# Optimization experiments

Measured on AMD Instinct MI355X. Metric: run time of the kernel, lower is better.

## Reference

```python
import jax, jax.numpy as jnp
import numpy as np


def _wkv_scan(key, value, time_decay, time_first):
    # Numerically-stabilized RWKV WKV recurrence; key/value: [B,T,C]
    w = -jnp.exp(time_decay)  # [C]
    B, T, C = key.shape

    def step(carry, kv):
        num, den, mx = carry
        k, v = kv  # [B,C] each
        # output at this timestep
        mo = jnp.maximum(mx, k + time_first)
        e1 = jnp.exp(mx - mo)
        e2 = jnp.exp(k + time_first - mo)
        out = (e1 * num + e2 * v) / (e1 * den + e2)
        # state update
        ms = jnp.maximum(mx + w, k)
        e1s = jnp.exp(mx + w - ms)
        e2s = jnp.exp(k - ms)
        return (e1s * num + e2s * v, e1s * den + e2s, ms), out

    init = (jnp.zeros((B, C), key.dtype),
            jnp.zeros((B, C), key.dtype),
            jnp.full((B, C), -1e38, key.dtype))
    kT = jnp.swapaxes(key, 0, 1)   # [T,B,C]
    vT = jnp.swapaxes(value, 0, 1)
    _, outs = jax.lax.scan(step, init, (kT, vT))
    return jnp.swapaxes(outs, 0, 1)  # [B,T,C]


def setup_inputs() -> dict:
    key = jax.random.key(0)
    ks = jax.random.split(key, 10)
    B, T, C = 8, 2048, 1024
    s = 1.0 / np.sqrt(C)
    return {
        "x": jax.random.normal(ks[0], (B, T, C), jnp.float32),
        "wk": jax.random.normal(ks[1], (C, C), jnp.float32) * s,
        "wv": jax.random.normal(ks[2], (C, C), jnp.float32) * s,
        "wr": jax.random.normal(ks[3], (C, C), jnp.float32) * s,
        "wo": jax.random.normal(ks[4], (C, C), jnp.float32) * s,
        "time_decay": jax.random.normal(ks[5], (C,), jnp.float32) * 0.5,
        "time_first": jax.random.normal(ks[6], (C,), jnp.float32) * 0.5,
        "mix_k": jax.random.uniform(ks[7], (1, 1, C), jnp.float32),
        "mix_v": jax.random.uniform(ks[8], (1, 1, C), jnp.float32),
        "mix_r": jax.random.uniform(ks[9], (1, 1, C), jnp.float32),
    }


def reference(x, wk, wv, wr, wo, time_decay, time_first, mix_k, mix_v, mix_r):
    # time_shift: prev_x[:,0]=0, prev_x[:,t]=x[:,t-1]  (ZeroPad2d((0,0,1,-1)))
    prev_x = jnp.pad(x, ((0, 0), (1, 0), (0, 0)))[:, :-1, :]
    k_in = x * mix_k + prev_x * (1.0 - mix_k)
    v_in = x * mix_v + prev_x * (1.0 - mix_v)
    r_in = x * mix_r + prev_x * (1.0 - mix_r)
    key = jnp.einsum('btc,dc->btd', k_in, wk)
    value = jnp.einsum('btc,dc->btd', v_in, wv)
    receptance = jax.nn.sigmoid(jnp.einsum('btc,dc->btd', r_in, wr))
    wkv = _wkv_scan(key, value, time_decay, time_first)
    rwkv = receptance * wkv
    return jnp.einsum('btc,dc->btd', rwkv, wo)
```

## Files before the change

kernel.cpp:

```cpp
#include <hip/hip_runtime.h>
#include <stdint.h>


using bf16x8 = __attribute__((ext_vector_type(8))) __bf16;
using f32x4  = __attribute__((ext_vector_type(4))) float;

union FU { float f; unsigned int u; };

__device__ __forceinline__ unsigned short f2b(float f) {
  FU v; v.f = f;
  unsigned int u = v.u;
  return (unsigned short)((u + 0x7fffu + ((u >> 16) & 1u)) >> 16);
}
__device__ __forceinline__ float b2f(unsigned short h) {
  FU v; v.u = ((unsigned int)h) << 16; return v.f;
}

__device__ __forceinline__ void gl_lds16(const unsigned short* g,
                                         const unsigned short* l) {
  __builtin_amdgcn_global_load_lds(
      (const __attribute__((address_space(1))) void*)g,
      (__attribute__((address_space(3))) void*)l, 16, 0, 0);
}

#define SBAR()  asm volatile("s_barrier" ::: "memory")
#define LGKMSOFT() asm volatile("s_waitcnt lgkmcnt(0)" ::: "memory")
#define VMW(n)  asm volatile("s_waitcnt vmcnt(" #n ")" ::: "memory")

__global__ __launch_bounds__(256) void prep_kernel(
    const float* __restrict__ x,
    const float* __restrict__ w0, const float* __restrict__ w1,
    const float* __restrict__ w2, const float* __restrict__ w3,
    unsigned short* __restrict__ o0, unsigned short* __restrict__ o1,
    unsigned short* __restrict__ o2, unsigned short* __restrict__ o3,
    const float* __restrict__ mk, const float* __restrict__ mv,
    const float* __restrict__ mr,
    unsigned short* __restrict__ ok, unsigned short* __restrict__ ov,
    unsigned short* __restrict__ orr, int T, int C)
{
  int bid = blockIdx.x;
  if (bid < 4096) {
    int mat = bid >> 10, blk = bid & 1023;
    const float* src = (mat == 0) ? w0 : (mat == 1) ? w1 : (mat == 2) ? w2 : w3;
    unsigned short* dst = (mat == 0) ? o0 : (mat == 1) ? o1 : (mat == 2) ? o2 : o3;
    int i = blk * 1024 + threadIdx.x * 4;
    float4 v = *(const float4*)(src + i);
    union { int2 i2; unsigned short u[4]; } o;
    o.u[0] = f2b(v.x); o.u[1] = f2b(v.y); o.u[2] = f2b(v.z); o.u[3] = f2b(v.w);
    *(int2*)(dst + i) = o.i2;
    return;
  }
  int i = (bid - 4096) * 256 + threadIdx.x;
  int base = i * 8;
  int row = base / C;
  int t = row - (row / T) * T;
  int c = base - row * C;
  float xv[8], pv[8];
  *(float4*)&xv[0] = *(const float4*)(x + base);
  *(float4*)&xv[4] = *(const float4*)(x + base + 4);
  if (t > 0) {
    *(float4*)&pv[0] = *(const float4*)(x + base - C);
    *(float4*)&pv[4] = *(const float4*)(x + base - C + 4);
  } else {
#pragma unroll
    for (int e = 0; e < 8; ++e) pv[e] = 0.f;
  }
  float mkv[8], mvv[8], mrv[8];
  *(float4*)&mkv[0] = *(const float4*)(mk + c);
  *(float4*)&mkv[4] = *(const float4*)(mk + c + 4);
  *(float4*)&mvv[0] = *(const float4*)(mv + c);
  *(float4*)&mvv[4] = *(const float4*)(mv + c + 4);
  *(float4*)&mrv[0] = *(const float4*)(mr + c);
  *(float4*)&mrv[4] = *(const float4*)(mr + c + 4);
  union { int4 i4; unsigned short u[8]; } a, b2, d;
#pragma unroll
  for (int e = 0; e < 8; ++e) {
    float xe = xv[e], pe = pv[e];
    a.u[e]  = f2b(xe * mkv[e] + pe * (1.f - mkv[e]));
    b2.u[e] = f2b(xe * mvv[e] + pe * (1.f - mvv[e]));
    d.u[e]  = f2b(xe * mrv[e] + pe * (1.f - mrv[e]));
  }
  *(int4*)(ok + base)  = a.i4;
  *(int4*)(ov + base)  = b2.i4;
  *(int4*)(orr + base) = d.i4;
}


__device__ __forceinline__ void stageHalf(
    const unsigned short* __restrict__ g,
    const unsigned short* l,
    int rh, int kt, int w, int rl, int koffel)
{
#pragma unroll
  for (int c = 0; c < 2; ++c) {
    int rows = rh * 128 + (2 * w + c) * 8;
    gl_lds16(g + (size_t)(rows + rl) * 1024 + kt * 64 + koffel,
             l + rows * 64);
  }
}

template<int Q>
__device__ __forceinline__ void quadMfma(f32x4 (&acc)[8][4],
    bf16x8 a00, bf16x8 a01, bf16x8 a10, bf16x8 a11, bf16x8 (&b)[4][2])
{
#pragma unroll
  for (int j = 0; j < 4; ++j) {
    acc[2*Q][j]   = __builtin_amdgcn_mfma_f32_16x16x32_bf16(a00, b[j][0], acc[2*Q][j],   0, 0, 0);
    acc[2*Q][j]   = __builtin_amdgcn_mfma_f32_16x16x32_bf16(a01, b[j][1], acc[2*Q][j],   0, 0, 0);
    acc[2*Q+1][j] = __builtin_amdgcn_mfma_f32_16x16x32_bf16(a10, b[j][0], acc[2*Q+1][j], 0, 0, 0);
    acc[2*Q+1][j] = __builtin_amdgcn_mfma_f32_16x16x32_bf16(a11, b[j][1], acc[2*Q+1][j], 0, 0, 0);
  }
}

template<bool ST_A, bool ST_B, int VMN>
__device__ __forceinline__ void ktile(
    const unsigned short* aR, const unsigned short* bR,
    const unsigned short* aW, const unsigned short* bW,
    const unsigned short* Am, const unsigned short* Wn,
    int ktA, int ktB, int w, int wm, int wn, int col, int quad,
    int swzel, int rl, int koffel, f32x4 (&acc)[8][4])
{
  const int ks0 = (quad * 8) ^ swzel;
  const int ks1 = (32 + quad * 8) ^ swzel;
  bf16x8 b[4][2];
#pragma unroll
  for (int j = 0; j < 4; ++j) {
    const unsigned short* br = bR + (wn * 64 + j * 16 + col) * 64;
    b[j][0] = *(const bf16x8*)(br + ks0);
    b[j][1] = *(const bf16x8*)(br + ks1);
  }
  const unsigned short* ar = aR + (wm * 128 + col) * 64;
  {
    bf16x8 a00 = *(const bf16x8*)(ar + 0 * 1024 + ks0);
    bf16x8 a01 = *(const bf16x8*)(ar + 0 * 1024 + ks1);
    bf16x8 a10 = *(const bf16x8*)(ar + 1 * 1024 + ks0);
    bf16x8 a11 = *(const bf16x8*)(ar + 1 * 1024 + ks1);
    if (ST_A) stageHalf(Am, aW, 0, ktA, w, rl, koffel);
    SBAR(); LGKMSOFT();
    __builtin_amdgcn_s_setprio(1);
    quadMfma<0>(acc, a00, a01, a10, a11, b);
    __builtin_amdgcn_s_setprio(0);
    SBAR();
  }
  {
    bf16x8 a00 = *(const bf16x8*)(ar + 2 * 1024 + ks0);
    bf16x8 a01 = *(const bf16x8*)(ar + 2 * 1024 + ks1);
    bf16x8 a10 = *(const bf16x8*)(ar + 3 * 1024 + ks0);
    bf16x8 a11 = *(const bf16x8*)(ar + 3 * 1024 + ks1);
    if (ST_A) stageHalf(Am, aW, 1, ktA, w, rl, koffel);
    SBAR(); LGKMSOFT();
    __builtin_amdgcn_s_setprio(1);
    quadMfma<1>(acc, a00, a01, a10, a11, b);
    __builtin_amdgcn_s_setprio(0);
    SBAR();
  }
  {
    bf16x8 a00 = *(const bf16x8*)(ar + 4 * 1024 + ks0);
    bf16x8 a01 = *(const bf16x8*)(ar + 4 * 1024 + ks1);
    bf16x8 a10 = *(const bf16x8*)(ar + 5 * 1024 + ks0);
    bf16x8 a11 = *(const bf16x8*)(ar + 5 * 1024 + ks1);
    if (ST_B) stageHalf(Wn, bW, 0, ktB, w, rl, koffel);
    SBAR(); LGKMSOFT();
    __builtin_amdgcn_s_setprio(1);
    quadMfma<2>(acc, a00, a01, a10, a11, b);
    __builtin_amdgcn_s_setprio(0);
    SBAR();
  }
  {
    bf16x8 a00 = *(const bf16x8*)(ar + 6 * 1024 + ks0);
    bf16x8 a01 = *(const bf16x8*)(ar + 6 * 1024 + ks1);
    bf16x8 a10 = *(const bf16x8*)(ar + 7 * 1024 + ks0);
    bf16x8 a11 = *(const bf16x8*)(ar + 7 * 1024 + ks1);
    if (ST_B) stageHalf(Wn, bW, 1, ktB, w, rl, koffel);
    SBAR(); LGKMSOFT();
    __builtin_amdgcn_s_setprio(1);
    quadMfma<3>(acc, a00, a01, a10, a11, b);
    __builtin_amdgcn_s_setprio(0);
    if constexpr (VMN == 4) { VMW(4); }
    else if constexpr (VMN == 0) { VMW(0); }
    SBAR();
  }
}

template<typename EPI>
__device__ __forceinline__ void gemm256(
    const unsigned short* __restrict__ A,
    const unsigned short* __restrict__ W,
    EPI epi)
{
  __shared__ __align__(16) unsigned short As[2][256 * 64];
  __shared__ __align__(16) unsigned short Bs[2][256 * 64];
  const int tid  = threadIdx.x;
  const int lane = tid & 63;
  const int w    = tid >> 6;
  const int wm   = w >> 2, wn = w & 3;
  const int col  = lane & 15, quad = lane >> 4;
  const int swzel  = (lane & 7) << 3;
  const int rl     = lane >> 3;
  const int koffel = ((lane & 7) ^ rl) << 3;
  const int mBase = blockIdx.x * 256;
  const int nBase = blockIdx.y * 256;
  const unsigned short* Am = A + (size_t)mBase * 1024;
  const unsigned short* Wn = W + (size_t)nBase * 1024;

  f32x4 acc[8][4];
  const f32x4 z = {0.f, 0.f, 0.f, 0.f};
#pragma unroll
  for (int i = 0; i < 8; ++i)
#pragma unroll
    for (int j = 0; j < 4; ++j) acc[i][j] = z;

  stageHalf(Wn, &Bs[0][0], 0, 0, w, rl, koffel);
  stageHalf(Wn, &Bs[0][0], 1, 0, w, rl, koffel);
  stageHalf(Am, &As[0][0], 0, 0, w, rl, koffel);
  stageHalf(Am, &As[0][0], 1, 0, w, rl, koffel);
  stageHalf(Wn, &Bs[1][0], 0, 1, w, rl, koffel);
  stageHalf(Wn, &Bs[1][0], 1, 1, w, rl, koffel);
  VMW(4); SBAR();

#pragma unroll 1
  for (int t = 0; t < 14; t += 2) {
    ktile<true, true, 4>(&As[0][0], &Bs[0][0], &As[1][0], &Bs[0][0],
                         Am, Wn, t + 1, t + 2,
                         w, wm, wn, col, quad, swzel, rl, koffel, acc);
    ktile<true, true, 4>(&As[1][0], &Bs[1][0], &As[0][0], &Bs[1][0],
                         Am, Wn, t + 2, t + 3,
                         w, wm, wn, col, quad, swzel, rl, koffel, acc);
  }
  ktile<true, false, 0>(&As[0][0], &Bs[0][0], &As[1][0], &Bs[0][0],
                        Am, Wn, 15, 0,
                        w, wm, wn, col, quad, swzel, rl, koffel, acc);
  ktile<false, false, -1>(&As[1][0], &Bs[1][0], &As[0][0], &Bs[1][0],
                          Am, Wn, 0, 0,
                          w, wm, wn, col, quad, swzel, rl, koffel, acc);

  const int mB = mBase + wm * 128, nB = nBase + wn * 64;
#pragma unroll
  for (int i = 0; i < 8; ++i)
#pragma unroll
    for (int j = 0; j < 4; ++j)
#pragma unroll
      for (int r = 0; r < 4; ++r)
        epi(mB + i * 16 + quad * 4 + r, nB + j * 16 + col, acc[i][j][r]);
}

__global__ __launch_bounds__(512, 2) void gemmKV2_kernel(
    const unsigned short* __restrict__ A0, const unsigned short* __restrict__ A1,
    const unsigned short* __restrict__ W0, const unsigned short* __restrict__ W1,
    unsigned short* __restrict__ out0, unsigned short* __restrict__ out1)
{
  const int z = blockIdx.z;
  const unsigned short* A = z ? A1 : A0;
  const unsigned short* W = z ? W1 : W0;
  unsigned short* out = z ? out1 : out0;
  gemm256(A, W, [&](int r, int c, float v) {
    out[(size_t)r * 1024 + c] = f2b(v);
  });
}

__global__ __launch_bounds__(512, 2) void gemmR2_kernel(
    const unsigned short* __restrict__ A, const unsigned short* __restrict__ W,
    unsigned short* __restrict__ out)
{
  gemm256(A, W, [&](int r, int c, float v) {
    out[(size_t)r * 1024 + c] = f2b(1.0f / (1.0f + __expf(-v)));
  });
}

__global__ __launch_bounds__(512, 2) void gemmO2_kernel(
    const unsigned short* __restrict__ A, const unsigned short* __restrict__ W,
    float* __restrict__ out)
{
  gemm256(A, W, [&](int r, int c, float v) {
    out[(size_t)r * 1024 + c] = v;
  });
}

__global__ __launch_bounds__(256) void wkv_pass1(
    const unsigned short* __restrict__ kb, const unsigned short* __restrict__ vb,
    const float* __restrict__ td,
    float* __restrict__ snum, float* __restrict__ sden, float* __restrict__ smx,
    int T, int C, int L)
{
  int g = blockIdx.x * 256 + threadIdx.x;
  int bc = g & 8191;
  int ch = g >> 13;
  int c = bc & 1023;
  float w = -__expf(td[c]);
  float num = 0.f, den = 0.f, mx = -1e38f;
  size_t base = ((size_t)(bc >> 10) * T + (size_t)ch * L) * C + c;
  for (int j0 = 0; j0 < L; j0 += 8) {
    float kq[8], vq[8];
#pragma unroll
    for (int j = 0; j < 8; ++j) {
      size_t a = base + (size_t)(j0 + j) * C;
      kq[j] = b2f(kb[a]);
      vq[j] = b2f(vb[a]);
    }
#pragma unroll
    for (int j = 0; j < 8; ++j) {
      float k = kq[j], v = vq[j];
      float mw = mx + w;
      float ms = fmaxf(mw, k);
      float s1 = __expf(mw - ms);
      float s2 = __expf(k - ms);
      num = s1 * num + s2 * v;
      den = s1 * den + s2;
      mx = ms;
    }
  }
  int idx = ch * 8192 + bc;
  snum[idx] = num; sden[idx] = den; smx[idx] = mx;
}

__global__ __launch_bounds__(64) void wkv_pass2(
    const float* __restrict__ snum, const float* __restrict__ sden,
    const float* __restrict__ smx, const float* __restrict__ td,
    float* __restrict__ inum, float* __restrict__ iden, float* __restrict__ imx,
    int L)
{
  int bc = blockIdx.x * 64 + threadIdx.x;
  int c = bc & 1023;
  float Wl = -__expf(td[c]) * (float)L;
  float num = 0.f, den = 0.f, mx = -1e38f;
#pragma unroll
  for (int ch = 0; ch < 32; ++ch) {
    int idx = ch * 8192 + bc;
    inum[idx] = num; iden[idx] = den; imx[idx] = mx;
    float sn = snum[idx], sd = sden[idx], sm = smx[idx];
    float mi = mx + Wl;
    float mo = fmaxf(mi, sm);
    float e1 = __expf(mi - mo);
    float e2 = __expf(sm - mo);
    num = e1 * num + e2 * sn;
    den = e1 * den + e2 * sd;
    mx = mo;
  }
}

__global__ __launch_bounds__(256) void wkv_pass3(
    const unsigned short* __restrict__ kb, const unsigned short* __restrict__ vb,
    const unsigned short* __restrict__ rsig,
    const float* __restrict__ td, const float* __restrict__ tf,
    const float* __restrict__ inum, const float* __restrict__ iden,
    const float* __restrict__ imx,
    unsigned short* __restrict__ rwkv, int T, int C, int L)
{
  int g = blockIdx.x * 256 + threadIdx.x;
  int bc = g & 8191;
  int ch = g >> 13;
  int c = bc & 1023;
  float w = -__expf(td[c]);
  float u = tf[c];
  int idx = ch * 8192 + bc;
  float num = inum[idx], den = iden[idx], mx = imx[idx];
  size_t base = ((size_t)(bc >> 10) * T + (size_t)ch * L) * C + c;
  for (int j0 = 0; j0 < L; j0 += 8) {
    float kq[8], vq[8], rq[8];
#pragma unroll
    for (int j = 0; j < 8; ++j) {
      size_t a = base + (size_t)(j0 + j) * C;
      kq[j] = b2f(kb[a]);
      vq[j] = b2f(vb[a]);
      rq[j] = b2f(rsig[a]);
    }
#pragma unroll
    for (int j = 0; j < 8; ++j) {
      float k = kq[j], v = vq[j];
      float ku = k + u;
      float mo = fmaxf(mx, ku);
      float e1 = __expf(mx - mo);
      float e2 = __expf(ku - mo);
      float o = (e1 * num + e2 * v) / (e1 * den + e2);
      rwkv[base + (size_t)(j0 + j) * C] = f2b(rq[j] * o);
      float mw = mx + w;
      float ms = fmaxf(mw, k);
      float s1 = __expf(mw - ms);
      float s2 = __expf(k - ms);
      num = s1 * num + s2 * v;
      den = s1 * den + s2;
      mx = ms;
    }
  }
}

extern "C" void kernel_launch(void* const* d_in, const int* in_sizes, int n_in,
                              void* d_out, int out_size, void* d_ws, size_t ws_size,
                              hipStream_t stream)
{
  const float* x  = (const float*)d_in[0];
  const float* wk = (const float*)d_in[1];
  const float* wv = (const float*)d_in[2];
  const float* wr = (const float*)d_in[3];
  const float* wo = (const float*)d_in[4];
  const float* td = (const float*)d_in[5];
  const float* tf = (const float*)d_in[6];
  const float* mk = (const float*)d_in[7];
  const float* mv = (const float*)d_in[8];
  const float* mr = (const float*)d_in[9];

  const int B = 8, T = 2048, C = 1024;
  const int M = B * T;
  const int NC = 32, L = 64;
  const size_t MB = 1024 * 1024;

  char* ws = (char*)d_ws;
  unsigned short* bufK = (unsigned short*)(ws);
  unsigned short* bufV = (unsigned short*)(ws + 32 * MB);
  unsigned short* bufR = (unsigned short*)(ws + 64 * MB);
  unsigned short* kb   = (unsigned short*)(ws + 96 * MB);
  unsigned short* wkb  = (unsigned short*)(ws + 128 * MB);
  unsigned short* wvb  = (unsigned short*)(ws + 130 * MB);
  unsigned short* wrb  = (unsigned short*)(ws + 132 * MB);
  unsigned short* wob  = (unsigned short*)(ws + 134 * MB);
  float* snum = (float*)(ws + 136 * MB);
  float* sden = (float*)(ws + 137 * MB);
  float* smx  = (float*)(ws + 138 * MB);
  float* inum = (float*)(ws + 139 * MB);
  float* iden = (float*)(ws + 140 * MB);
  float* imx  = (float*)(ws + 141 * MB);
  unsigned short* vb   = (unsigned short*)(ws + 142 * MB);
  unsigned short* rsig = bufV;
  unsigned short* rwkv = bufR;

  dim3 gKV(M / 256, C / 256, 2);
  dim3 gG(M / 256, C / 256);
  int scanBlocks = (B * C * NC) / 256;

  prep_kernel<<<12288, 256, 0, stream>>>(x, wk, wv, wr, wo, wkb, wvb, wrb, wob,
                                         mk, mv, mr, bufK, bufV, bufR, T, C);
  gemmKV2_kernel<<<gKV, 512, 0, stream>>>(bufK, bufV, wkb, wvb, kb, vb);
  gemmR2_kernel<<<gG, 512, 0, stream>>>(bufR, wrb, rsig);
  wkv_pass1<<<scanBlocks, 256, 0, stream>>>(kb, vb, td, snum, sden, smx, T, C, L);
  wkv_pass2<<<(B * C) / 64, 64, 0, stream>>>(snum, sden, smx, td, inum, iden, imx, L);
  wkv_pass3<<<scanBlocks, 256, 0, stream>>>(kb, vb, rsig, td, tf, inum, iden, imx,
                                            rwkv, T, C, L);
  gemmO2_kernel<<<gG, 512, 0, stream>>>(rwkv, wob, (float*)d_out);
}
```

Baseline: 333.1 us.

## Prefetch A fragments one quarter ahead and vectorize WKV scan over 4 channels

The GEMM k-tile now loads the next quarter's A fragments from LDS before issuing the current quarter's MFMAs, and drops the explicit lgkmcnt(0) wait, so LDS reads can overlap with matrix math. The WKV scan passes now have each thread handle 4 adjacent channels through 8-byte vector loads and stores, and the chunk length changes from 64 to 32 (64 chunks), which gives more parallel chunks but fewer threads overall. The chunk-state buffers move to the start of the workspace, and the prefetching raises register pressure in the GEMM.

```diff
diff --git a/kernel.cpp b/kernel.cpp
--- a/kernel.cpp
+++ b/kernel.cpp
@@ -24,7 +24,6 @@
 }
 
 #define SBAR()  asm volatile("s_barrier" ::: "memory")
-#define LGKMSOFT() asm volatile("s_waitcnt lgkmcnt(0)" ::: "memory")
 #define VMW(n)  asm volatile("s_waitcnt vmcnt(" #n ")" ::: "memory")
 
 __global__ __launch_bounds__(256) void prep_kernel(
@@ -122,6 +121,13 @@
 {
   const int ks0 = (quad * 8) ^ swzel;
   const int ks1 = (32 + quad * 8) ^ swzel;
+  const unsigned short* ar = aR + (wm * 128 + col) * 64;
+
+  bf16x8 a0[4], a1[4];
+  a0[0] = *(const bf16x8*)(ar + 0 * 1024 + ks0);
+  a0[1] = *(const bf16x8*)(ar + 0 * 1024 + ks1);
+  a0[2] = *(const bf16x8*)(ar + 1 * 1024 + ks0);
+  a0[3] = *(const bf16x8*)(ar + 1 * 1024 + ks1);
   bf16x8 b[4][2];
 #pragma unroll
   for (int j = 0; j < 4; ++j) {
@@ -129,57 +135,46 @@
     b[j][0] = *(const bf16x8*)(br + ks0);
     b[j][1] = *(const bf16x8*)(br + ks1);
   }
-  const unsigned short* ar = aR + (wm * 128 + col) * 64;
-  {
-    bf16x8 a00 = *(const bf16x8*)(ar + 0 * 1024 + ks0);
-    bf16x8 a01 = *(const bf16x8*)(ar + 0 * 1024 + ks1);
-    bf16x8 a10 = *(const bf16x8*)(ar + 1 * 1024 + ks0);
-    bf16x8 a11 = *(const bf16x8*)(ar + 1 * 1024 + ks1);
-    if (ST_A) stageHalf(Am, aW, 0, ktA, w, rl, koffel);
-    SBAR(); LGKMSOFT();
-    __builtin_amdgcn_s_setprio(1);
-    quadMfma<0>(acc, a00, a01, a10, a11, b);
-    __builtin_amdgcn_s_setprio(0);
-    SBAR();
-  }
-  {
-    bf16x8 a00 = *(const bf16x8*)(ar + 2 * 1024 + ks0);
-    bf16x8 a01 = *(const bf16x8*)(ar + 2 * 1024 + ks1);
-    bf16x8 a10 = *(const bf16x8*)(ar + 3 * 1024 + ks0);
-    bf16x8 a11 = *(const bf16x8*)(ar + 3 * 1024 + ks1);
-    if (ST_A) stageHalf(Am, aW, 1, ktA, w, rl, koffel);
-    SBAR(); LGKMSOFT();
-    __builtin_amdgcn_s_setprio(1);
-    quadMfma<1>(acc, a00, a01, a10, a11, b);
-    __builtin_amdgcn_s_setprio(0);
-    SBAR();
-  }
-  {
-    bf16x8 a00 = *(const bf16x8*)(ar + 4 * 1024 + ks0);
-    bf16x8 a01 = *(const bf16x8*)(ar + 4 * 1024 + ks1);
-    bf16x8 a10 = *(const bf16x8*)(ar + 5 * 1024 + ks0);
-    bf16x8 a11 = *(const bf16x8*)(ar + 5 * 1024 + ks1);
-    if (ST_B) stageHalf(Wn, bW, 0, ktB, w, rl, koffel);
-    SBAR(); LGKMSOFT();
-    __builtin_amdgcn_s_setprio(1);
-    quadMfma<2>(acc, a00, a01, a10, a11, b);
-    __builtin_amdgcn_s_setprio(0);
-    SBAR();
-  }
-  {
-    bf16x8 a00 = *(const bf16x8*)(ar + 6 * 1024 + ks0);
-    bf16x8 a01 = *(const bf16x8*)(ar + 6 * 1024 + ks1);
-    bf16x8 a10 = *(const bf16x8*)(ar + 7 * 1024 + ks0);
-    bf16x8 a11 = *(const bf16x8*)(ar + 7 * 1024 + ks1);
-    if (ST_B) stageHalf(Wn, bW, 1, ktB, w, rl, koffel);
-    SBAR(); LGKMSOFT();
-    __builtin_amdgcn_s_setprio(1);
-    quadMfma<3>(acc, a00, a01, a10, a11, b);
-    __builtin_amdgcn_s_setprio(0);
-    if constexpr (VMN == 4) { VMW(4); }
-    else if constexpr (VMN == 0) { VMW(0); }
-    SBAR();
-  }
+  a1[0] = *(const bf16x8*)(ar + 2 * 1024 + ks0);
+  a1[1] = *(const bf16x8*)(ar + 2 * 1024 + ks1);
+  a1[2] = *(const bf16x8*)(ar + 3 * 1024 + ks0);
+  a1[3] = *(const bf16x8*)(ar + 3 * 1024 + ks1);
+  if (ST_A) stageHalf(Am, aW, 0, ktA, w, rl, koffel);
+  SBAR();
+  __builtin_amdgcn_s_setprio(1);
+  quadMfma<0>(acc, a0[0], a0[1], a0[2], a0[3], b);
+  __builtin_amdgcn_s_setprio(0);
+  SBAR();
+  bf16x8 a2[4];
+  a2[0] = *(const bf16x8*)(ar + 4 * 1024 + ks0);
+  a2[1] = *(const bf16x8*)(ar + 4 * 1024 + ks1);
+  a2[2] = *(const bf16x8*)(ar + 5 * 1024 + ks0);
+  a2[3] = *(const bf16x8*)(ar + 5 * 1024 + ks1);
+  if (ST_A) stageHalf(Am, aW, 1, ktA, w, rl, koffel);
+  SBAR();
+  __builtin_amdgcn_s_setprio(1);
+  quadMfma<1>(acc, a1[0], a1[1], a1[2], a1[3], b);
+  __builtin_amdgcn_s_setprio(0);
+  SBAR();
+  bf16x8 a3[4];
+  a3[0] = *(const bf16x8*)(ar + 6 * 1024 + ks0);
+  a3[1] = *(const bf16x8*)(ar + 6 * 1024 + ks1);
+  a3[2] = *(const bf16x8*)(ar + 7 * 1024 + ks0);
+  a3[3] = *(const bf16x8*)(ar + 7 * 1024 + ks1);
+  if (ST_B) stageHalf(Wn, bW, 0, ktB, w, rl, koffel);
+  SBAR();
+  __builtin_amdgcn_s_setprio(1);
+  quadMfma<2>(acc, a2[0], a2[1], a2[2], a2[3], b);
+  __builtin_amdgcn_s_setprio(0);
+  SBAR();
+  if (ST_B) stageHalf(Wn, bW, 1, ktB, w, rl, koffel);
+  SBAR();
+  __builtin_amdgcn_s_setprio(1);
+  quadMfma<3>(acc, a3[0], a3[1], a3[2], a3[3], b);
+  __builtin_amdgcn_s_setprio(0);
+  if constexpr (VMN == 4) { VMW(4); }
+  else if constexpr (VMN == 0) { VMW(0); }
+  SBAR();
 }
 
 template<typename EPI>
@@ -276,55 +271,72 @@
   });
 }
 
+__device__ __forceinline__ void unpack4(uint2 u, float* f) {
+  f[0] = b2f((unsigned short)(u.x & 0xffffu));
+  f[1] = b2f((unsigned short)(u.x >> 16));
+  f[2] = b2f((unsigned short)(u.y & 0xffffu));
+  f[3] = b2f((unsigned short)(u.y >> 16));
+}
+
 __global__ __launch_bounds__(256) void wkv_pass1(
     const unsigned short* __restrict__ kb, const unsigned short* __restrict__ vb,
     const float* __restrict__ td,
     float* __restrict__ snum, float* __restrict__ sden, float* __restrict__ smx,
-    int T, int C, int L)
+    int T, int C)
 {
   int g = blockIdx.x * 256 + threadIdx.x;
-  int bc = g & 8191;
-  int ch = g >> 13;
-  int c = bc & 1023;
-  float w = -__expf(td[c]);
-  float num = 0.f, den = 0.f, mx = -1e38f;
-  size_t base = ((size_t)(bc >> 10) * T + (size_t)ch * L) * C + c;
-  for (int j0 = 0; j0 < L; j0 += 8) {
-    float kq[8], vq[8];
+  int cq = g & 255;
+  int rest = g >> 8;
+  int ch = rest & 63;
+  int b  = rest >> 6;
+  int c0 = cq * 4;
+  float4 td4 = *(const float4*)(td + c0);
+  float w[4] = {-__expf(td4.x), -__expf(td4.y), -__expf(td4.z), -__expf(td4.w)};
+  float num[4] = {0.f, 0.f, 0.f, 0.f};
+  float den[4] = {0.f, 0.f, 0.f, 0.f};
+  float mx[4]  = {-1e38f, -1e38f, -1e38f, -1e38f};
+  size_t base = ((size_t)b * T + (size_t)ch * 32) * C + c0;
+  for (int j0 = 0; j0 < 32; j0 += 8) {
+    uint2 kq[8], vq[8];
 #pragma unroll
     for (int j = 0; j < 8; ++j) {
       size_t a = base + (size_t)(j0 + j) * C;
-      kq[j] = b2f(kb[a]);
-      vq[j] = b2f(vb[a]);
+      kq[j] = *(const uint2*)(kb + a);
+      vq[j] = *(const uint2*)(vb + a);
     }
 #pragma unroll
     for (int j = 0; j < 8; ++j) {
-      float k = kq[j], v = vq[j];
-      float mw = mx + w;
-      float ms = fmaxf(mw, k);
-      float s1 = __expf(mw - ms);
-      float s2 = __expf(k - ms);
-      num = s1 * num + s2 * v;
-      den = s1 * den + s2;
-      mx = ms;
+      float kf[4], vf[4];
+      unpack4(kq[j], kf); unpack4(vq[j], vf);
+#pragma unroll
+      for (int e = 0; e < 4; ++e) {
+        float mw = mx[e] + w[e];
+        float ms = fmaxf(mw, kf[e]);
+        float s1 = __expf(mw - ms);
+        float s2 = __expf(kf[e] - ms);
+        num[e] = s1 * num[e] + s2 * vf[e];
+        den[e] = s1 * den[e] + s2;
+        mx[e] = ms;
+      }
     }
   }
-  int idx = ch * 8192 + bc;
-  snum[idx] = num; sden[idx] = den; smx[idx] = mx;
+  int idx = ch * 8192 + b * 1024 + c0;
+  *(float4*)(snum + idx) = make_float4(num[0], num[1], num[2], num[3]);
+  *(float4*)(sden + idx) = make_float4(den[0], den[1], den[2], den[3]);
+  *(float4*)(smx  + idx) = make_float4(mx[0], mx[1], mx[2], mx[3]);
 }
 
 __global__ __launch_bounds__(64) void wkv_pass2(
     const float* __restrict__ snum, const float* __restrict__ sden,
     const float* __restrict__ smx, const float* __restrict__ td,
-    float* __restrict__ inum, float* __restrict__ iden, float* __restrict__ imx,
-    int L)
+    float* __restrict__ inum, float* __restrict__ iden, float* __restrict__ imx)
 {
   int bc = blockIdx.x * 64 + threadIdx.x;
   int c = bc & 1023;
-  float Wl = -__expf(td[c]) * (float)L;
+  float Wl = -__expf(td[c]) * 32.0f;
   float num = 0.f, den = 0.f, mx = -1e38f;
 #pragma unroll
-  for (int ch = 0; ch < 32; ++ch) {
+  for (int ch = 0; ch < 64; ++ch) {
     int idx = ch * 8192 + bc;
     inum[idx] = num; iden[idx] = den; imx[idx] = mx;
     float sn = snum[idx], sd = sden[idx], sm = smx[idx];
@@ -344,42 +356,57 @@
     const float* __restrict__ td, const float* __restrict__ tf,
     const float* __restrict__ inum, const float* __restrict__ iden,
     const float* __restrict__ imx,
-    unsigned short* __restrict__ rwkv, int T, int C, int L)
+    unsigned short* __restrict__ rwkv, int T, int C)
 {
   int g = blockIdx.x * 256 + threadIdx.x;
-  int bc = g & 8191;
-  int ch = g >> 13;
-  int c = bc & 1023;
-  float w = -__expf(td[c]);
-  float u = tf[c];
-  int idx = ch * 8192 + bc;
-  float num = inum[idx], den = iden[idx], mx = imx[idx];
-  size_t base = ((size_t)(bc >> 10) * T + (size_t)ch * L) * C + c;
-  for (int j0 = 0; j0 < L; j0 += 8) {
-    float kq[8], vq[8], rq[8];
+  int cq = g & 255;
+  int rest = g >> 8;
+  int ch = rest & 63;
+  int b  = rest >> 6;
+  int c0 = cq * 4;
+  float4 td4 = *(const float4*)(td + c0);
+  float4 tf4 = *(const float4*)(tf + c0);
+  float w[4] = {-__expf(td4.x), -__expf(td4.y), -__expf(td4.z), -__expf(td4.w)};
+  float u[4] = {tf4.x, tf4.y, tf4.z, tf4.w};
+  int idx = ch * 8192 + b * 1024 + c0;
+  float4 n4 = *(const float4*)(inum + idx);
+  float4 d4 = *(const float4*)(iden + idx);
+  float4 m4 = *(const float4*)(imx + idx);
+  float num[4] = {n4.x, n4.y, n4.z, n4.w};
+  float den[4] = {d4.x, d4.y, d4.z, d4.w};
+  float mx[4]  = {m4.x, m4.y, m4.z, m4.w};
+  size_t base = ((size_t)b * T + (size_t)ch * 32) * C + c0;
+  for (int j0 = 0; j0 < 32; j0 += 8) {
+    uint2 kq[8], vq[8], rq[8];
 #pragma unroll
     for (int j = 0; j < 8; ++j) {
       size_t a = base + (size_t)(j0 + j) * C;
-      kq[j] = b2f(kb[a]);
-      vq[j] = b2f(vb[a]);
-      rq[j] = b2f(rsig[a]);
+      kq[j] = *(const uint2*)(kb + a);
+      vq[j] = *(const uint2*)(vb + a);
+      rq[j] = *(const uint2*)(rsig + a);
     }
 #pragma unroll
     for (int j = 0; j < 8; ++j) {
-      float k = kq[j], v = vq[j];
-      float ku = k + u;
-      float mo = fmaxf(mx, ku);
-      float e1 = __expf(mx - mo);
-      float e2 = __expf(ku - mo);
-      float o = (e1 * num + e2 * v) / (e1 * den + e2);
-      rwkv[base + (size_t)(j0 + j) * C] = f2b(rq[j] * o);
-      float mw = mx + w;
-      float ms = fmaxf(mw, k);
-      float s1 = __expf(mw - ms);
-      float s2 = __expf(k - ms);
-      num = s1 * num + s2 * v;
-      den = s1 * den + s2;
-      mx = ms;
+      float kf[4], vf[4], rf[4];
+      unpack4(kq[j], kf); unpack4(vq[j], vf); unpack4(rq[j], rf);
+      union { uint2 u2; unsigned short s[4]; } o;
+#pragma unroll
+      for (int e = 0; e < 4; ++e) {
+        float ku = kf[e] + u[e];
+        float mo = fmaxf(mx[e], ku);
+        float e1 = __expf(mx[e] - mo);
+        float e2 = __expf(ku - mo);
+        float out = (e1 * num[e] + e2 * vf[e]) / (e1 * den[e] + e2);
+        o.s[e] = f2b(rf[e] * out);
+        float mw = mx[e] + w[e];
+        float ms = fmaxf(mw, kf[e]);
+        float s1 = __expf(mw - ms);
+        float s2 = __expf(kf[e] - ms);
+        num[e] = s1 * num[e] + s2 * vf[e];
+        den[e] = s1 * den[e] + s2;
+        mx[e] = ms;
+      }
+      *(uint2*)(rwkv + base + (size_t)(j0 + j) * C) = o.u2;
     }
   }
 }
@@ -401,7 +428,6 @@
 
   const int B = 8, T = 2048, C = 1024;
   const int M = B * T;
-  const int NC = 32, L = 64;
   const size_t MB = 1024 * 1024;
 
   char* ws = (char*)d_ws;
@@ -413,27 +439,26 @@
   unsigned short* wvb  = (unsigned short*)(ws + 130 * MB);
   unsigned short* wrb  = (unsigned short*)(ws + 132 * MB);
   unsigned short* wob  = (unsigned short*)(ws + 134 * MB);
-  float* snum = (float*)(ws + 136 * MB);
-  float* sden = (float*)(ws + 137 * MB);
-  float* smx  = (float*)(ws + 138 * MB);
-  float* inum = (float*)(ws + 139 * MB);
-  float* iden = (float*)(ws + 140 * MB);
-  float* imx  = (float*)(ws + 141 * MB);
   unsigned short* vb   = (unsigned short*)(ws + 142 * MB);
+  float* snum = (float*)(ws + 0 * MB);
+  float* sden = (float*)(ws + 2 * MB);
+  float* smx  = (float*)(ws + 4 * MB);
+  float* inum = (float*)(ws + 6 * MB);
+  float* iden = (float*)(ws + 8 * MB);
+  float* imx  = (float*)(ws + 10 * MB);
   unsigned short* rsig = bufV;
   unsigned short* rwkv = bufR;
 
   dim3 gKV(M / 256, C / 256, 2);
   dim3 gG(M / 256, C / 256);
-  int scanBlocks = (B * C * NC) / 256;
 
   prep_kernel<<<12288, 256, 0, stream>>>(x, wk, wv, wr, wo, wkb, wvb, wrb, wob,
                                          mk, mv, mr, bufK, bufV, bufR, T, C);
   gemmKV2_kernel<<<gKV, 512, 0, stream>>>(bufK, bufV, wkb, wvb, kb, vb);
   gemmR2_kernel<<<gG, 512, 0, stream>>>(bufR, wrb, rsig);
-  wkv_pass1<<<scanBlocks, 256, 0, stream>>>(kb, vb, td, snum, sden, smx, T, C, L);
-  wkv_pass2<<<(B * C) / 64, 64, 0, stream>>>(snum, sden, smx, td, inum, iden, imx, L);
-  wkv_pass3<<<scanBlocks, 256, 0, stream>>>(kb, vb, rsig, td, tf, inum, iden, imx,
-                                            rwkv, T, C, L);
+  wkv_pass1<<<512, 256, 0, stream>>>(kb, vb, td, snum, sden, smx, T, C);
+  wkv_pass2<<<128, 64, 0, stream>>>(snum, sden, smx, td, inum, iden, imx);
+  wkv_pass3<<<512, 256, 0, stream>>>(kb, vb, rsig, td, tf, inum, iden, imx,
+                                     rwkv, T, C);
   gemmO2_kernel<<<gG, 512, 0, stream>>>(rwkv, wob, (float*)d_out);
 }
```

After: 345.0 us. +3.6%, slower.
